# Optimization experiments

Measured on AMD Instinct MI355X. Metric: run time of the kernel, lower is better.

Reference implementation:

```python
import jax, jax.numpy as jnp
from jax import lax
import numpy as np

B, T, F = 32, 512, 512
NUM_OUTPUTS = 23   # joints
DEV_CLASSES = 8
# layer specs: (input_dim, units)
LAYERS = [(F, 1024), (1024, 128), (128, NUM_OUTPUTS),
          (128 + NUM_OUTPUTS, 256), (256, 128), (128, DEV_CLASSES)]


def _gru_params(key, fan_in, units):
    k1, k2, k3 = jax.random.split(key, 3)
    kernel = jax.random.normal(k1, (fan_in, 3 * units), jnp.float32) / jnp.sqrt(jnp.float32(fan_in))
    rkernel = jax.random.normal(k2, (units, 3 * units), jnp.float32) * jnp.float32(0.02)
    bias = jnp.zeros((2, 3 * units), jnp.float32)  # [input_bias, recurrent_bias] (reset_after=True)
    return kernel, rkernel, bias


def setup_inputs() -> dict:
    key = jax.random.key(0)
    keys = jax.random.split(key, 7)
    inp = {"x": jax.random.normal(keys[0], (B, T, F), jnp.float32)}
    for i, (fi, u) in enumerate(LAYERS):
        k, r, b = _gru_params(keys[i + 1], fi, u)
        inp[f"k{i+1}"] = k
        inp[f"r{i+1}"] = r
        inp[f"b{i+1}"] = b
    return inp


def gru(x, kernel, rkernel, bias, act):
    """Keras GRU, reset_after=True, recurrent_activation=sigmoid, gate order z|r|h.
    x: [B,T,F]; kernel: [F,3U]; rkernel: [U,3U]; bias: [2,3U]. Returns [B,T,U]."""
    units = rkernel.shape[0]
    b_i, b_r = bias[0], bias[1]
    # precompute input projections for all timesteps (one big GEMM)
    xp = jnp.einsum('btf,fg->btg', x, kernel) + b_i  # [B,T,3U]

    def step(h, xt):
        rp = h @ rkernel + b_r                       # [B,3U]
        xz, xr, xh = jnp.split(xt, 3, axis=-1)
        rz, rr, rh = jnp.split(rp, 3, axis=-1)
        z = jax.nn.sigmoid(xz + rz)
        r = jax.nn.sigmoid(xr + rr)
        hh = act(xh + r * rh)                        # reset applied AFTER recurrent matmul
        h_new = z * h + (1.0 - z) * hh
        return h_new, h_new

    h0 = jnp.zeros((x.shape[0], units), x.dtype)
    _, ys = lax.scan(step, h0, jnp.swapaxes(xp, 0, 1))  # scan over time
    return jnp.swapaxes(ys, 0, 1)                        # [B,T,U]


relu = jax.nn.relu
linear = lambda v: v


def reference(x, k1, r1, b1, k2, r2, b2, k3, r3, b3,
              k4, r4, b4, k5, r5, b5, k6, r6, b6):
    z = gru(x, k1, r1, b1, relu)          # tcn_gru1: 1024
    z1 = gru(z, k2, r2, b2, relu)         # tcn_gru2: 128
    ye = gru(z1, k3, r3, b3, linear)      # tcn_dgru: num_outputs
    yc = jnp.concatenate([z1, ye], axis=-1)
    y = gru(yc, k4, r4, b4, relu)         # dev_gru1: 256
    y = gru(y, k5, r5, b5, relu)          # dev_gru2: 128
    yd = gru(y, k6, r6, b6, linear)       # dev_dgru: dev_classes
    return ye, yd
```

## Files before the change

kernel.cpp:

```cpp
#include <hip/hip_runtime.h>
#include <hip/hip_bf16.h>
#include <cstdint>
#include <cstddef>

#define BB 32
#define TT 512

typedef short s8v __attribute__((ext_vector_type(8)));
typedef float f4v __attribute__((ext_vector_type(4)));
typedef unsigned long long u64;
typedef unsigned short u16;
typedef unsigned int u32;

__device__ __forceinline__ short f2b(float x) {
  __hip_bfloat16 h = __float2bfloat16(x);
  return *reinterpret_cast<short*>(&h);
}
__device__ __forceinline__ float b2f(u16 x) {
  __hip_bfloat16 h = *reinterpret_cast<__hip_bfloat16*>(&x);
  return __bfloat162float(h);
}
__device__ __forceinline__ float sigm(float x) { return 1.f / (1.f + __expf(-x)); }

__device__ __forceinline__ f4v load16_sc(const void* p) {
  f4v v;
  asm volatile("global_load_dwordx4 %0, %1, off sc0 sc1" : "=v"(v) : "v"(p));
  return v;
}
__device__ __forceinline__ void vm_wait0() {
  asm volatile("s_waitcnt vmcnt(0)" ::: "memory");
}
__device__ __forceinline__ u32 ldP(const u32* p) {
  return __hip_atomic_load(p, __ATOMIC_RELAXED, __HIP_MEMORY_SCOPE_AGENT);
}
__device__ __forceinline__ void stP(u32* p, u32 v) {
  __hip_atomic_store(p, v, __ATOMIC_RELEASE, __HIP_MEMORY_SCOPE_AGENT);
}
__device__ __forceinline__ void stW(u32* p, u32 v) {
  __hip_atomic_store(p, v, __ATOMIC_RELAXED, __HIP_MEMORY_SCOPE_AGENT);
}
__device__ __forceinline__ u32 ldW(const u32* p) {
  return __hip_atomic_load(p, __ATOMIC_RELAXED, __HIP_MEMORY_SCOPE_AGENT);
}

__device__ __forceinline__ void waitP(u32* flags, int baseA, int na, u32 thA,
                                      int baseB, int nbb, u32 thB,
                                      int baseS, int ns, u32 thS) {
  const int tid = threadIdx.x;
  for (;;) {
    int ok = 1;
    if (tid < na) ok = (ldP(&flags[(baseA + tid) * 32]) >= thA) ? 1 : 0;
    else if (tid < na + nbb) ok = (ldP(&flags[(baseB + tid - na) * 32]) >= thB) ? 1 : 0;
    else if (tid < na + nbb + ns) ok = (ldP(&flags[(baseS + tid - na - nbb) * 32]) >= thS) ? 1 : 0;
    if (__syncthreads_count(ok) == (int)blockDim.x) break;
    __builtin_amdgcn_s_sleep(1);
  }
}

__global__ __launch_bounds__(256) void cast_bf16(const float* __restrict__ in,
                                                 u16* __restrict__ outp, int n4) {
  int i = blockIdx.x * 256 + threadIdx.x;
  if (i < n4) {
    float4 v = *(const float4*)(in + (size_t)i * 4);
    u16 o[4] = {(u16)f2b(v.x), (u16)f2b(v.y), (u16)f2b(v.z), (u16)f2b(v.w)};
    *(u64*)(outp + (size_t)i * 4) = *(const u64*)o;
  }
}

__global__ __launch_bounds__(256) void prep_frags(const float* __restrict__ src,
                                                  u16* __restrict__ dst,
                                                  int N, int Ksrc, int Ks,
                                                  int JT, int U, int recmode, int total_fid) {
  int t = blockIdx.x * 256 + threadIdx.x;
  int lane = t & 63, fid = t >> 6;
  if (fid >= total_fid) return;
  int l15 = lane & 15, quad = lane >> 4;
  int ks = fid % Ks;
  int n, valid_n;
  if (recmode) {
    int rest = fid / Ks;
    int jt = rest % JT;
    int g = rest / JT;
    int jj = jt * 16 + l15;
    n = g * U + jj;
    valid_n = (jj < U) ? 1 : 0;
  } else {
    int nt = fid / Ks;
    n = nt * 16 + l15;
    valid_n = (n < N) ? 1 : 0;
  }
  u16* o = dst + ((size_t)fid * 64 + lane) * 8;
#pragma unroll
  for (int j = 0; j < 8; ++j) {
    int k = ks * 32 + quad * 8 + j;
    float v = (valid_n && k < Ksrc) ? src[(size_t)k * N + n] : 0.f;
    o[j] = (u16)f2b(v);
  }
}

__global__ __launch_bounds__(256) void prep_comb(const float* __restrict__ Kmat,
                                                 const float* __restrict__ Rmat,
                                                 u16* __restrict__ dst,
                                                 int N, int U, int w1v, int w1p,
                                                 int w2v, int w2p, int Ks, int JT,
                                                 int total_fid) {
  int t = blockIdx.x * 256 + threadIdx.x;
  int lane = t & 63, fid = t >> 6;
  if (fid >= total_fid) return;
  int l15 = lane & 15, quad = lane >> 4;
  int ks = fid % Ks;
  int rest = fid / Ks;
  int jt = rest % JT;
  int g = rest / JT;
  int j = jt * 16 + l15;
  bool jv = (j < U);
  int n = g * U + (jv ? j : 0);
  u16* o = dst + ((size_t)fid * 64 + lane) * 8;
#pragma unroll
  for (int jj = 0; jj < 8; ++jj) {
    int k = ks * 32 + quad * 8 + jj;
    float v = 0.f;
    if (jv) {
      if (k < w1p) {
        if (k < w1v) v = Kmat[(size_t)k * N + n];
      } else if (k < w1p + w2p) {
        int kr = k - w1p;
        if (kr < w2v) v = Kmat[(size_t)(w1v + kr) * N + n];
      } else {
        int rr = k - w1p - w2p;
        if (rr < U) v = Rmat[(size_t)rr * N + n];
      }
    }
    o[jj] = (u16)f2b(v);
  }
}

__global__ __launch_bounds__(256) void gemm_mfma(const u16* __restrict__ A, int strideA, int Kact,
                                                 const u16* __restrict__ Bf,
                                                 const float* __restrict__ bias,
                                                 float* __restrict__ C,
                                                 int N, int Ntiles, int Ks,
                                                 int t0, int tcLog2) {
  __shared__ char sha[16 * 2056];
  const int tid = threadIdx.x;
  const int lane = tid & 63, l15 = lane & 15, quad = lane >> 4, w = tid >> 6;
  const int KS4 = Ks * 8;
  const int rowB = Ks * 64 + 8;
  const int bm = blockIdx.y * 16;

  for (int i = tid; i < 16 * KS4; i += 256) {
    int r = i / KS4, u = i - r * KS4;
    u64 v = 0;
    if (u * 4 < Kact) {
      int rl = bm + r;
      size_t grow;
      if (t0 >= 0) {
        int tcm = (1 << tcLog2) - 1;
        grow = (((size_t)(rl >> tcLog2)) << 9) + t0 + (rl & tcm);
      } else {
        grow = (size_t)rl;
      }
      v = *((const u64*)(A + grow * (size_t)strideA) + u);
    }
    *(u64*)(sha + r * rowB + u * 8) = v;
  }
  __syncthreads();

  f4v acc[4];
  f4v z4 = {0.f, 0.f, 0.f, 0.f};
#pragma unroll
  for (int q = 0; q < 4; ++q) acc[q] = z4;

  const int ntb = blockIdx.x * 16 + w * 4;
  for (int ks = 0; ks < Ks; ++ks) {
    int off = l15 * rowB + ks * 64 + quad * 16;
    s8v a = *(const s8v*)(sha + off);
#pragma unroll
    for (int q = 0; q < 4; ++q) {
      int nt = ntb + q;
      if (nt < Ntiles) {
        s8v b = *(const s8v*)(Bf + (((size_t)nt * Ks + ks) * 64 + lane) * 8);
        acc[q] = __builtin_amdgcn_mfma_f32_16x16x32_bf16(a, b, acc[q], 0, 0, 0);
      }
    }
  }
#pragma unroll
  for (int q = 0; q < 4; ++q) {
    int nt = ntb + q;
    if (nt >= Ntiles) continue;
    int col = nt * 16 + l15;
    if (col < N) {
      float bv = bias[col];
#pragma unroll
      for (int r = 0; r < 4; ++r) {
        int rowl = bm + quad * 4 + r;
        C[(size_t)rowl * N + col] = acc[q][r] + bv;
      }
    }
  }
}

struct GCfg {
  const u16 *s1, *s2;
  const u16* Bf;
  const float* bias;
  u16* ydst;
  float* fdst;
  u16* hglob;
  int w1p, w2p, Upad, U, Ks, ksIn, JT, nb, base, act, wfd;
  int baseA, na, baseB, nbb;
};

#define SMEM_BYTES 91648
#define HPOFF 74240

__device__ __attribute__((noinline)) void stage_l1(
    const float* xp, const u16* Bf, const float* brec, u16* hbuf, u16* yout,
    u32* flags, int t0, int tc, char* smem) {
  const int tid = threadIdx.x;
  const int lane = tid & 63, l15 = lane & 15, quad = (lane >> 4) & 3;
  const int w = tid >> 6;
  const int blk = blockIdx.x;
  const int jt = blk * 8 + (w & 7);
  const int Mt = w >> 3;
  const int j = jt * 16 + l15;
  const int HP = 32 * 1024;

  const float bz = brec[j], brr = brec[1024 + j], bh = brec[2048 + j];
  float hprev[4];
  {
    const u32* hp = (const u32*)(hbuf + (size_t)(t0 & 1) * HP);
#pragma unroll
    for (int r = 0; r < 4; ++r) {
      int b = Mt * 16 + quad * 4 + r;
      u32 wd = ldW(hp + ((b * 1024 + (j & ~1)) >> 1));
      hprev[r] = b2f((j & 1) ? (u16)(wd >> 16) : (u16)(wd & 0xffff));
    }
  }

  for (int tt = 0; tt < tc; ++tt) {
    const int t = t0 + tt;
    waitP(flags, 0, 8, (u32)t, 0, 0, 0, 0, 0, 0);
    float xv[3][4];
#pragma unroll
    for (int r = 0; r < 4; ++r) {
      int b = Mt * 16 + quad * 4 + r;
      const float* xr_ = xp + ((size_t)b * tc + tt) * 3072;
      xv[0][r] = __builtin_nontemporal_load(xr_ + j);
      xv[1][r] = __builtin_nontemporal_load(xr_ + 1024 + j);
      xv[2][r] = __builtin_nontemporal_load(xr_ + 2048 + j);
    }
    {
      const char* hsrc = (const char*)(hbuf + (size_t)(t & 1) * HP);
      f4v vals[4];
#pragma unroll
      for (int i = 0; i < 4; ++i)
        vals[i] = load16_sc(hsrc + (size_t)(tid + i * 1024) * 16);
      vm_wait0();
#pragma unroll
      for (int i = 0; i < 4; ++i) {
        int g16 = tid + i * 1024;
        *(f4v*)(smem + (g16 >> 7) * 2064 + (g16 & 127) * 16) = vals[i];
      }
    }
    __syncthreads();
    f4v acc[3];
    f4v z4 = {0.f, 0.f, 0.f, 0.f};
#pragma unroll
    for (int g = 0; g < 3; ++g) acc[g] = z4;
#pragma unroll 4
    for (int ks = 0; ks < 32; ++ks) {
      s8v a = *(const s8v*)(smem + (Mt * 16 + l15) * 2064 + ks * 64 + quad * 16);
#pragma unroll
      for (int g = 0; g < 3; ++g) {
        s8v b = *(const s8v*)(Bf + (((size_t)(g * 64 + jt) * 32 + ks) * 64 + lane) * 8);
        acc[g] = __builtin_amdgcn_mfma_f32_16x16x32_bf16(a, b, acc[g], 0, 0, 0);
      }
    }
    u16* hdst = hbuf + (size_t)((t + 1) & 1) * HP;
#pragma unroll
    for (int r = 0; r < 4; ++r) {
      int b = Mt * 16 + quad * 4 + r;
      size_t row = (size_t)b * tc + tt;
      float z = sigm(xv[0][r] + acc[0][r] + bz);
      float rr = sigm(xv[1][r] + acc[1][r] + brr);
      float hh = fmaxf(xv[2][r] + rr * (acc[2][r] + bh), 0.f);
      float hnew = z * hprev[r] + (1.f - z) * hh;
      hprev[r] = hnew;
      float part = __shfl_xor(hnew, 1, 64);
      if ((l15 & 1) == 0) {
        u32 wd = (u32)(u16)f2b(hnew) | ((u32)(u16)f2b(part) << 16);
        stW((u32*)hdst + ((b * 1024 + j) >> 1), wd);
        stW((u32*)yout + ((row * 1024 + j) >> 1), wd);
      }
    }
    __syncthreads();
    if (tid == 0) stP(&flags[blk * 32], (u32)(t + 1));
  }
}

__device__ __attribute__((noinline)) void stage_gen(
    const GCfg& c, int bs, u32* flags, int t0, int tc, int initH, char* smem) {
  const int tid = threadIdx.x;
  const int lane = tid & 63, l15 = lane & 15, quad = (lane >> 4) & 3;
  const int w = tid >> 6;
  const int Kc = c.w1p + c.w2p + c.Upad;
  const int rowA = Kc * 2 + 16;
  const int rowH = c.Upad * 2 + 16;
  char* Ab = smem;
  char* Hp = smem + HPOFF;
  const int HB = 32 * rowH;
  const int uIn = (c.w1p + c.w2p) >> 3;
  const int uH = c.Upad >> 3;
  const int upr = uIn + ((c.nb > 1) ? uH : 0);
  const int total_units = 32 * upr;
  const int u1 = c.w1p >> 3;
  const int U = c.U;
  const int HPstride = 32 * c.Upad;

  const int ntask = c.JT * 2;
  int tcount = 0;
  int tjt[2], tmt[2];
#pragma unroll
  for (int i = 0; i < 2; ++i) {
    int task = w * c.nb + bs + i * 16 * c.nb;
    if (task < ntask) { tjt[tcount] = task >> 1; tmt[tcount] = task & 1; ++tcount; }
  }

  const float* b0 = c.bias;
  const float* b1 = c.bias + 3 * U;
  float bz[2], br_[2], bih[2], brh[2];
  int jl[2];
  bool jv[2];
#pragma unroll
  for (int i = 0; i < 2; ++i) {
    if (i >= tcount) { jv[i] = false; jl[i] = 0; bz[i] = br_[i] = bih[i] = brh[i] = 0.f; continue; }
    int j = tjt[i] * 16 + l15;
    jv[i] = (j < U);
    int jc = jv[i] ? j : 0;
    jl[i] = j;
    bz[i] = b0[jc] + b1[jc];
    br_[i] = b0[U + jc] + b1[U + jc];
    bih[i] = b0[2 * U + jc];
    brh[i] = b1[2 * U + jc];
  }

  if (c.nb == 1) {
    for (int i = tid; i < (2 * HB) >> 2; i += 1024) ((u32*)Hp)[i] = 0;
    __syncthreads();
    if (!initH) {
      for (int i = tid; i < 32 * uH; i += 1024) {
        int m = i / uH, u = i - m * uH;
        *(f4v*)(Hp + (t0 & 1) * HB + m * rowH + u * 16) = *((const f4v*)c.hglob + i);
      }
    }
    __syncthreads();
  }

  float hprev[2][4];
#pragma unroll
  for (int i = 0; i < 2; ++i) {
    if (i >= tcount) continue;
#pragma unroll
    for (int r = 0; r < 4; ++r) {
      int b = tmt[i] * 16 + quad * 4 + r;
      float hv;
      if (c.nb > 1) {
        u32 wd = ldW((const u32*)c.hglob + (((t0 & 1) * HPstride + b * c.Upad + (jl[i] & ~1)) >> 1));
        hv = b2f((jl[i] & 1) ? (u16)(wd >> 16) : (u16)(wd & 0xffff));
      } else {
        hv = b2f(*(const u16*)(Hp + (t0 & 1) * HB + b * rowH + jl[i] * 2));
      }
      hprev[i][r] = jv[i] ? hv : 0.f;
    }
  }

  for (int tt = 0; tt < tc; ++tt) {
    const int t = t0 + tt;
    waitP(flags, c.baseA, c.na, (u32)(t + 1), c.baseB, c.nbb, (u32)(t + 1),
          c.base, (c.nb > 1) ? c.nb : 0, (u32)t);
    {
      f4v vals[5];
      int offs[5];
#pragma unroll
      for (int i = 0; i < 5; ++i) {
        int idx = tid + i * 1024;
        int pidx = (idx < total_units) ? idx : (total_units - 1);
        int m = pidx / upr, u = pidx - m * upr;
        const char* src;
        if (u < u1)
          src = (const char*)c.s1 + ((size_t)(m * tc + tt) * c.w1p + (u << 3)) * 2;
        else if (u < uIn)
          src = (const char*)c.s2 + ((size_t)(m * tc + tt) * c.w2p + ((u - u1) << 3)) * 2;
        else
          src = (const char*)c.hglob + ((size_t)(t & 1) * HPstride + m * c.Upad + ((u - uIn) << 3)) * 2;
        vals[i] = load16_sc(src);
        offs[i] = m * rowA + u * 16;
      }
      vm_wait0();
#pragma unroll
      for (int i = 0; i < 5; ++i)
        if (tid + i * 1024 < total_units) *(f4v*)(Ab + offs[i]) = vals[i];
    }
    __syncthreads();
    f4v az[2], ar[2], axh[2], arh[2];
    f4v z4 = {0.f, 0.f, 0.f, 0.f};
#pragma unroll
    for (int i = 0; i < 2; ++i) { az[i] = z4; ar[i] = z4; axh[i] = z4; arh[i] = z4; }
    for (int ks = 0; ks < c.ksIn; ++ks) {
#pragma unroll
      for (int i = 0; i < 2; ++i) {
        if (i >= tcount) break;
        s8v a = *(const s8v*)(Ab + (tmt[i] * 16 + l15) * rowA + ks * 64 + quad * 16);
        const u16* bb = c.Bf + ((size_t)tjt[i] * c.Ks + ks) * 512 + lane * 8;
        s8v bz_ = *(const s8v*)(bb);
        s8v br2 = *(const s8v*)(bb + (size_t)c.JT * c.Ks * 512);
        s8v bh2 = *(const s8v*)(bb + (size_t)2 * c.JT * c.Ks * 512);
        az[i] = __builtin_amdgcn_mfma_f32_16x16x32_bf16(a, bz_, az[i], 0, 0, 0);
        ar[i] = __builtin_amdgcn_mfma_f32_16x16x32_bf16(a, br2, ar[i], 0, 0, 0);
        axh[i] = __builtin_amdgcn_mfma_f32_16x16x32_bf16(a, bh2, axh[i], 0, 0, 0);
      }
    }
    for (int ks = c.ksIn; ks < c.Ks; ++ks) {
#pragma unroll
      for (int i = 0; i < 2; ++i) {
        if (i >= tcount) break;
        s8v a;
        if (c.nb > 1)
          a = *(const s8v*)(Ab + (tmt[i] * 16 + l15) * rowA + ks * 64 + quad * 16);
        else
          a = *(const s8v*)(Hp + (t & 1) * HB + (tmt[i] * 16 + l15) * rowH + (ks - c.ksIn) * 64 + quad * 16);
        const u16* bb = c.Bf + ((size_t)tjt[i] * c.Ks + ks) * 512 + lane * 8;
        s8v bz_ = *(const s8v*)(bb);
        s8v br2 = *(const s8v*)(bb + (size_t)c.JT * c.Ks * 512);
        s8v bh2 = *(const s8v*)(bb + (size_t)2 * c.JT * c.Ks * 512);
        az[i] = __builtin_amdgcn_mfma_f32_16x16x32_bf16(a, bz_, az[i], 0, 0, 0);
        ar[i] = __builtin_amdgcn_mfma_f32_16x16x32_bf16(a, br2, ar[i], 0, 0, 0);
        arh[i] = __builtin_amdgcn_mfma_f32_16x16x32_bf16(a, bh2, arh[i], 0, 0, 0);
      }
    }
#pragma unroll
    for (int i = 0; i < 2; ++i) {
      if (i >= tcount) break;
#pragma unroll
      for (int r = 0; r < 4; ++r) {
        int b = tmt[i] * 16 + quad * 4 + r;
        size_t row = (size_t)b * tc + tt;
        float z = sigm(az[i][r] + bz[i]);
        float rg = sigm(ar[i][r] + br_[i]);
        float hh = axh[i][r] + bih[i] + rg * (arh[i][r] + brh[i]);
        if (c.act) hh = fmaxf(hh, 0.f);
        float hnew = z * hprev[i][r] + (1.f - z) * hh;
        if (!jv[i]) hnew = 0.f;
        hprev[i][r] = hnew;
        int j = jl[i];
        float part = __shfl_xor(hnew, 1, 64);
        u32 wd = (u32)(u16)f2b(hnew) | ((u32)(u16)f2b(part) << 16);
        if ((l15 & 1) == 0) {
          if (c.ydst) stW((u32*)c.ydst + ((row * c.Upad + j) >> 1), wd);
          if (c.nb > 1)
            stW((u32*)c.hglob + ((((t + 1) & 1) * HPstride + b * c.Upad + j) >> 1), wd);
        }
        if (c.nb == 1) *(u16*)(Hp + ((t + 1) & 1) * HB + b * rowH + j * 2) = (u16)f2b(hnew);
        if (c.fdst && jv[i] && j < c.wfd)
          c.fdst[((size_t)b * TT + t) * c.wfd + j] = hnew;
      }
    }
    __syncthreads();
    if (tid == 0) stP(&flags[(c.base + bs) * 32], (u32)(t + 1));
  }
  if (c.nb == 1) {
    int pf = (t0 + tc) & 1;
    for (int i = tid; i < 32 * uH; i += 1024) {
      int m = i / uH, u = i - m * uH;
      *((f4v*)c.hglob + i) = *(const f4v*)(Hp + pf * HB + m * rowH + u * 16);
    }
  }
}

__global__ __launch_bounds__(1024, 1) void pipeline(
    const float* xp, const u16* BfL1, const float* brecL1, u16* hbufL1, u16* y1c,
    GCfg c1, GCfg c2, GCfg c3, GCfg c4, GCfg c5,
    u32* flags, int t0, int tc, int initH) {
  __shared__ char smem[SMEM_BYTES];
  int blk = blockIdx.x;
  if (blk < 8) stage_l1(xp, BfL1, brecL1, hbufL1, y1c, flags, t0, tc, smem);
  else if (blk < 10) stage_gen(c1, blk - 8, flags, t0, tc, initH, smem);
  else if (blk < 11) stage_gen(c2, 0, flags, t0, tc, initH, smem);
  else if (blk < 13) stage_gen(c3, blk - 11, flags, t0, tc, initH, smem);
  else if (blk < 14) stage_gen(c4, 0, flags, t0, tc, initH, smem);
  else stage_gen(c5, 0, flags, t0, tc, initH, smem);
}

extern "C" void kernel_launch(void* const* d_in, const int* in_sizes, int n_in,
                              void* d_out, int out_size, void* d_ws, size_t ws_size,
                              hipStream_t stream) {
  const float* x = (const float*)d_in[0];

  int tcLog2 = 6;
  {
    size_t fixed = (size_t)16384 * 512 * 2
                   + (3145728ull + 1572864ull + 442368 + 15360 + 319488 + 147456 + 7680) * 2
                   + 300000;
    for (; tcLog2 >= 4; --tcLog2) {
      size_t rc = (size_t)BB << tcLog2;
      size_t per = rc * 3072 * 4 + rc * (1024 + 128 + 32 + 256 + 128) * 2 + 8192;
      if (fixed + per <= ws_size || tcLog2 == 4) break;
    }
  }
  const int Tc = 1 << tcLog2;
  const int NCk = TT / Tc;
  const size_t RC = (size_t)BB * Tc;

  char* ws = (char*)d_ws;
  size_t off = 0;
  auto alloc = [&](size_t bytes) -> char* {
    char* p = ws + off;
    off += (bytes + 255) & ~(size_t)255;
    return p;
  };

  u32* flags = (u32*)alloc(15 * 32 * sizeof(u32));
  u16* hbufL1 = (u16*)alloc((size_t)2 * 32 * 1024 * 2);
  u16* hb2 = (u16*)alloc((size_t)2 * 32 * 128 * 2);
  u16* hb4 = (u16*)alloc((size_t)2 * 32 * 256 * 2);
  u16* hs3 = (u16*)alloc((size_t)32 * 32 * 2);
  u16* hs5 = (u16*)alloc((size_t)32 * 128 * 2);
  u16* hs6 = (u16*)alloc((size_t)32 * 32 * 2);
  u16* recB1 = (u16*)alloc(3145728ull * 2);
  u16* gemB1 = (u16*)alloc(1572864ull * 2);
  u16* cB[5];
  const size_t cBe[5] = {442368, 15360, 319488, 147456, 7680};
  for (int i = 0; i < 5; ++i) cB[i] = (u16*)alloc(cBe[i] * 2);
  u16* x16 = (u16*)alloc((size_t)16384 * 512 * 2);
  float* xp = (float*)alloc(RC * 3072 * sizeof(float));
  u16* y1c = (u16*)alloc(RC * 1024 * 2);
  u16* y2c = (u16*)alloc(RC * 128 * 2);
  u16* yec = (u16*)alloc(RC * 32 * 2);
  u16* y4c = (u16*)alloc(RC * 256 * 2);
  u16* y5c = (u16*)alloc(RC * 128 * 2);

  float* outye = (float*)d_out;
  float* outyd = outye + (size_t)BB * TT * 23;

  hipMemsetAsync(flags, 0, 15 * 32 * sizeof(u32), stream);
  hipMemsetAsync(hbufL1, 0, (size_t)2 * 32 * 1024 * 2, stream);
  hipMemsetAsync(hb2, 0, (size_t)2 * 32 * 128 * 2, stream);
  hipMemsetAsync(hb4, 0, (size_t)2 * 32 * 256 * 2, stream);

  {
    int n4 = (16384 * 512) / 4;
    hipLaunchKernelGGL(cast_bf16, dim3((n4 + 255) / 256), dim3(256), 0, stream, x, x16, n4);
    hipLaunchKernelGGL(prep_frags, dim3((3 * 64 * 32 * 64 + 255) / 256), dim3(256), 0, stream,
                       (const float*)d_in[2], recB1, 3072, 1024, 32, 64, 1024, 1, 3 * 64 * 32);
    hipLaunchKernelGGL(prep_frags, dim3((192 * 16 * 64 + 255) / 256), dim3(256), 0, stream,
                       (const float*)d_in[1], gemB1, 3072, 512, 16, 0, 0, 0, 192 * 16);
    const int pc[5][8] = {
        {384, 128, 1024, 1024, 0, 0, 36, 8},
        {69, 23, 128, 128, 0, 0, 5, 2},
        {768, 256, 128, 128, 23, 32, 13, 16},
        {384, 128, 256, 256, 0, 0, 12, 8},
        {24, 8, 128, 128, 0, 0, 5, 1}};
    for (int i = 0; i < 5; ++i) {
      int l = i + 1;
      int tf = 3 * pc[i][7] * pc[i][6];
      hipLaunchKernelGGL(prep_comb, dim3((tf * 64 + 255) / 256), dim3(256), 0, stream,
                         (const float*)d_in[1 + 3 * l], (const float*)d_in[2 + 3 * l], cB[i],
                         pc[i][0], pc[i][1], pc[i][2], pc[i][3], pc[i][4], pc[i][5],
                         pc[i][6], pc[i][7], tf);
    }
  }

  GCfg c1 = {y1c, nullptr, cB[0], (const float*)d_in[6], y2c, nullptr, hb2,
             1024, 0, 128, 128, 36, 32, 8, 2, 8, 1, 0, 0, 8, 0, 0};
  GCfg c2 = {y2c, nullptr, cB[1], (const float*)d_in[9], yec, outye, hs3,
             128, 0, 32, 23, 5, 4, 2, 1, 10, 0, 23, 8, 2, 0, 0};
  GCfg c3 = {y2c, yec, cB[2], (const float*)d_in[12], y4c, nullptr, hb4,
             128, 32, 256, 256, 13, 5, 16, 2, 11, 1, 0, 8, 2, 10, 1};
  GCfg c4 = {y4c, nullptr, cB[3], (const float*)d_in[15], y5c, nullptr, hs5,
             256, 0, 128, 128, 12, 8, 8, 1, 13, 1, 0, 11, 2, 0, 0};
  GCfg c5 = {y5c, nullptr, cB[4], (const float*)d_in[18], nullptr, outyd, hs6,
             128, 0, 32, 8, 5, 4, 1, 1, 14, 0, 8, 13, 1, 0, 0};

  const float* biasL1 = (const float*)d_in[3];

  for (int c = 0; c < NCk; ++c) {
    const int t0 = c * Tc;
    hipLaunchKernelGGL(gemm_mfma, dim3(12, (unsigned)(RC / 16)), dim3(256), 0, stream,
                       x16, 512, 512, gemB1, biasL1, xp, 3072, 192, 16, t0, tcLog2);
    hipLaunchKernelGGL(pipeline, dim3(15), dim3(1024), 0, stream,
                       xp, recB1, biasL1 + 3072, hbufL1, y1c,
                       c1, c2, c3, c4, c5, flags, t0, Tc, (c == 0) ? 1 : 0);
  }
}
```

Baseline: 15.34 ms.

## Spread GRU pipeline stages over more workgroups with split-K reduction in layer 1

Layer-1 recurrence moves from 8 to 32 workgroups, each owning two 16-column tiles, with the K dimension split across four wave groups and partial sums reduced through shared memory. Downstream stages also get more blocks (c1 8, c3 8, c4 4), and the grid grows to 54 blocks with matching flag/config updates. The flag wait now polls with a single wavefront and then does a block barrier. The aim is to cut per-timestep latency of the serial recurrence by spreading the per-step matmul over more CUs. The cost is more cross-block synchronisation per step, an extra shared-memory reduction, and a larger per-block shared allocation.

```diff
diff --git a/kernel.cpp b/kernel.cpp
--- a/kernel.cpp
+++ b/kernel.cpp
@@ -47,14 +47,17 @@
                                       int baseB, int nbb, u32 thB,
                                       int baseS, int ns, u32 thS) {
   const int tid = threadIdx.x;
-  for (;;) {
-    int ok = 1;
-    if (tid < na) ok = (ldP(&flags[(baseA + tid) * 32]) >= thA) ? 1 : 0;
-    else if (tid < na + nbb) ok = (ldP(&flags[(baseB + tid - na) * 32]) >= thB) ? 1 : 0;
-    else if (tid < na + nbb + ns) ok = (ldP(&flags[(baseS + tid - na - nbb) * 32]) >= thS) ? 1 : 0;
-    if (__syncthreads_count(ok) == (int)blockDim.x) break;
-    __builtin_amdgcn_s_sleep(1);
-  }
+  if (tid < 64) {
+    for (;;) {
+      int ok = 1;
+      if (tid < na) ok = (ldP(&flags[(baseA + tid) * 32]) >= thA) ? 1 : 0;
+      else if (tid < na + nbb) ok = (ldP(&flags[(baseB + tid - na) * 32]) >= thB) ? 1 : 0;
+      else if (tid < na + nbb + ns) ok = (ldP(&flags[(baseS + tid - na - nbb) * 32]) >= thS) ? 1 : 0;
+      if (__all(ok)) break;
+      __builtin_amdgcn_s_sleep(1);
+    }
+  }
+  __syncthreads();
 }
 
 __global__ __launch_bounds__(256) void cast_bf16(const float* __restrict__ in,
@@ -211,7 +214,8 @@
   int baseA, na, baseB, nbb;
 };
 
-#define SMEM_BYTES 91648
+#define REDOFF 66048
+#define SMEM_BYTES 102912
 #define HPOFF 74240
 
 __device__ __attribute__((noinline)) void stage_l1(
@@ -220,15 +224,19 @@
   const int tid = threadIdx.x;
   const int lane = tid & 63, l15 = lane & 15, quad = (lane >> 4) & 3;
   const int w = tid >> 6;
+  const int kq = w >> 2;
+  const int jt_l = (w >> 1) & 1;
+  const int Mt = w & 1;
   const int blk = blockIdx.x;
-  const int jt = blk * 8 + (w & 7);
-  const int Mt = w >> 3;
+  const int jt = blk * 2 + jt_l;
   const int j = jt * 16 + l15;
   const int HP = 32 * 1024;
-
-  const float bz = brec[j], brr = brec[1024 + j], bh = brec[2048 + j];
+  const bool own = (kq == 0);
+
+  float bz = 0.f, brr = 0.f, bh = 0.f;
   float hprev[4];
-  {
+  if (own) {
+    bz = brec[j]; brr = brec[1024 + j]; bh = brec[2048 + j];
     const u32* hp = (const u32*)(hbuf + (size_t)(t0 & 1) * HP);
 #pragma unroll
     for (int r = 0; r < 4; ++r) {
@@ -240,15 +248,17 @@
 
   for (int tt = 0; tt < tc; ++tt) {
     const int t = t0 + tt;
-    waitP(flags, 0, 8, (u32)t, 0, 0, 0, 0, 0, 0);
+    waitP(flags, 0, 32, (u32)t, 0, 0, 0, 0, 0, 0);
     float xv[3][4];
-#pragma unroll
-    for (int r = 0; r < 4; ++r) {
-      int b = Mt * 16 + quad * 4 + r;
-      const float* xr_ = xp + ((size_t)b * tc + tt) * 3072;
-      xv[0][r] = __builtin_nontemporal_load(xr_ + j);
-      xv[1][r] = __builtin_nontemporal_load(xr_ + 1024 + j);
-      xv[2][r] = __builtin_nontemporal_load(xr_ + 2048 + j);
+    if (own) {
+#pragma unroll
+      for (int r = 0; r < 4; ++r) {
+        int b = Mt * 16 + quad * 4 + r;
+        const float* xr_ = xp + ((size_t)b * tc + tt) * 3072;
+        xv[0][r] = __builtin_nontemporal_load(xr_ + j);
+        xv[1][r] = __builtin_nontemporal_load(xr_ + 1024 + j);
+        xv[2][r] = __builtin_nontemporal_load(xr_ + 2048 + j);
+      }
     }
     {
       const char* hsrc = (const char*)(hbuf + (size_t)(t & 1) * HP);
@@ -268,8 +278,9 @@
     f4v z4 = {0.f, 0.f, 0.f, 0.f};
 #pragma unroll
     for (int g = 0; g < 3; ++g) acc[g] = z4;
-#pragma unroll 4
-    for (int ks = 0; ks < 32; ++ks) {
+#pragma unroll
+    for (int i = 0; i < 8; ++i) {
+      int ks = kq * 8 + i;
       s8v a = *(const s8v*)(smem + (Mt * 16 + l15) * 2064 + ks * 64 + quad * 16);
 #pragma unroll
       for (int g = 0; g < 3; ++g) {
@@ -277,21 +288,37 @@
         acc[g] = __builtin_amdgcn_mfma_f32_16x16x32_bf16(a, b, acc[g], 0, 0, 0);
       }
     }
-    u16* hdst = hbuf + (size_t)((t + 1) & 1) * HP;
-#pragma unroll
-    for (int r = 0; r < 4; ++r) {
-      int b = Mt * 16 + quad * 4 + r;
-      size_t row = (size_t)b * tc + tt;
-      float z = sigm(xv[0][r] + acc[0][r] + bz);
-      float rr = sigm(xv[1][r] + acc[1][r] + brr);
-      float hh = fmaxf(xv[2][r] + rr * (acc[2][r] + bh), 0.f);
-      float hnew = z * hprev[r] + (1.f - z) * hh;
-      hprev[r] = hnew;
-      float part = __shfl_xor(hnew, 1, 64);
-      if ((l15 & 1) == 0) {
-        u32 wd = (u32)(u16)f2b(hnew) | ((u32)(u16)f2b(part) << 16);
-        stW((u32*)hdst + ((b * 1024 + j) >> 1), wd);
-        stW((u32*)yout + ((row * 1024 + j) >> 1), wd);
+    if (!own) {
+      int idx = (kq - 1) * 4 + (w & 3);
+#pragma unroll
+      for (int g = 0; g < 3; ++g)
+        *(f4v*)(smem + REDOFF + ((g * 12 + idx) * 64 + lane) * 16) = acc[g];
+    }
+    __syncthreads();
+    if (own) {
+#pragma unroll
+      for (int g = 0; g < 3; ++g)
+#pragma unroll
+        for (int kk = 0; kk < 3; ++kk) {
+          f4v p = *(const f4v*)(smem + REDOFF + ((g * 12 + kk * 4 + w) * 64 + lane) * 16);
+          acc[g] += p;
+        }
+      u16* hdst = hbuf + (size_t)((t + 1) & 1) * HP;
+#pragma unroll
+      for (int r = 0; r < 4; ++r) {
+        int b = Mt * 16 + quad * 4 + r;
+        size_t row = (size_t)b * tc + tt;
+        float z = sigm(xv[0][r] + acc[0][r] + bz);
+        float rr = sigm(xv[1][r] + acc[1][r] + brr);
+        float hh = fmaxf(xv[2][r] + rr * (acc[2][r] + bh), 0.f);
+        float hnew = z * hprev[r] + (1.f - z) * hh;
+        hprev[r] = hnew;
+        float part = __shfl_xor(hnew, 1, 64);
+        if ((l15 & 1) == 0) {
+          u32 wd = (u32)(u16)f2b(hnew) | ((u32)(u16)f2b(part) << 16);
+          stW((u32*)hdst + ((b * 1024 + j) >> 1), wd);
+          stW((u32*)yout + ((row * 1024 + j) >> 1), wd);
+        }
       }
     }
     __syncthreads();
@@ -484,11 +511,11 @@
     u32* flags, int t0, int tc, int initH) {
   __shared__ char smem[SMEM_BYTES];
   int blk = blockIdx.x;
-  if (blk < 8) stage_l1(xp, BfL1, brecL1, hbufL1, y1c, flags, t0, tc, smem);
-  else if (blk < 10) stage_gen(c1, blk - 8, flags, t0, tc, initH, smem);
-  else if (blk < 11) stage_gen(c2, 0, flags, t0, tc, initH, smem);
-  else if (blk < 13) stage_gen(c3, blk - 11, flags, t0, tc, initH, smem);
-  else if (blk < 14) stage_gen(c4, 0, flags, t0, tc, initH, smem);
+  if (blk < 32) stage_l1(xp, BfL1, brecL1, hbufL1, y1c, flags, t0, tc, smem);
+  else if (blk < 40) stage_gen(c1, blk - 32, flags, t0, tc, initH, smem);
+  else if (blk < 41) stage_gen(c2, 0, flags, t0, tc, initH, smem);
+  else if (blk < 49) stage_gen(c3, blk - 41, flags, t0, tc, initH, smem);
+  else if (blk < 53) stage_gen(c4, blk - 49, flags, t0, tc, initH, smem);
   else stage_gen(c5, 0, flags, t0, tc, initH, smem);
 }
 
@@ -520,12 +547,12 @@
     return p;
   };
 
-  u32* flags = (u32*)alloc(15 * 32 * sizeof(u32));
+  u32* flags = (u32*)alloc(54 * 32 * sizeof(u32));
   u16* hbufL1 = (u16*)alloc((size_t)2 * 32 * 1024 * 2);
   u16* hb2 = (u16*)alloc((size_t)2 * 32 * 128 * 2);
   u16* hb4 = (u16*)alloc((size_t)2 * 32 * 256 * 2);
+  u16* hb5 = (u16*)alloc((size_t)2 * 32 * 128 * 2);
   u16* hs3 = (u16*)alloc((size_t)32 * 32 * 2);
-  u16* hs5 = (u16*)alloc((size_t)32 * 128 * 2);
   u16* hs6 = (u16*)alloc((size_t)32 * 32 * 2);
   u16* recB1 = (u16*)alloc(3145728ull * 2);
   u16* gemB1 = (u16*)alloc(1572864ull * 2);
@@ -543,10 +570,11 @@
   float* outye = (float*)d_out;
   float* outyd = outye + (size_t)BB * TT * 23;
 
-  hipMemsetAsync(flags, 0, 15 * 32 * sizeof(u32), stream);
+  hipMemsetAsync(flags, 0, 54 * 32 * sizeof(u32), stream);
   hipMemsetAsync(hbufL1, 0, (size_t)2 * 32 * 1024 * 2, stream);
   hipMemsetAsync(hb2, 0, (size_t)2 * 32 * 128 * 2, stream);
   hipMemsetAsync(hb4, 0, (size_t)2 * 32 * 256 * 2, stream);
+  hipMemsetAsync(hb5, 0, (size_t)2 * 32 * 128 * 2, stream);
 
   {
     int n4 = (16384 * 512) / 4;
@@ -572,15 +600,15 @@
   }
 
   GCfg c1 = {y1c, nullptr, cB[0], (const float*)d_in[6], y2c, nullptr, hb2,
-             1024, 0, 128, 128, 36, 32, 8, 2, 8, 1, 0, 0, 8, 0, 0};
+             1024, 0, 128, 128, 36, 32, 8, 8, 32, 1, 0, 0, 32, 0, 0};
   GCfg c2 = {y2c, nullptr, cB[1], (const float*)d_in[9], yec, outye, hs3,
-             128, 0, 32, 23, 5, 4, 2, 1, 10, 0, 23, 8, 2, 0, 0};
+             128, 0, 32, 23, 5, 4, 2, 1, 40, 0, 23, 32, 8, 0, 0};
   GCfg c3 = {y2c, yec, cB[2], (const float*)d_in[12], y4c, nullptr, hb4,
-             128, 32, 256, 256, 13, 5, 16, 2, 11, 1, 0, 8, 2, 10, 1};
-  GCfg c4 = {y4c, nullptr, cB[3], (const float*)d_in[15], y5c, nullptr, hs5,
-             256, 0, 128, 128, 12, 8, 8, 1, 13, 1, 0, 11, 2, 0, 0};
+             128, 32, 256, 256, 13, 5, 16, 8, 41, 1, 0, 32, 8, 40, 1};
+  GCfg c4 = {y4c, nullptr, cB[3], (const float*)d_in[15], y5c, nullptr, hb5,
+             256, 0, 128, 128, 12, 8, 8, 4, 49, 1, 0, 41, 8, 0, 0};
   GCfg c5 = {y5c, nullptr, cB[4], (const float*)d_in[18], nullptr, outyd, hs6,
-             128, 0, 32, 8, 5, 4, 1, 1, 14, 0, 8, 13, 1, 0, 0};
+             128, 0, 32, 8, 5, 4, 1, 1, 53, 0, 8, 49, 4, 0, 0};
 
   const float* biasL1 = (const float*)d_in[3];
 
@@ -588,7 +616,7 @@
     const int t0 = c * Tc;
     hipLaunchKernelGGL(gemm_mfma, dim3(12, (unsigned)(RC / 16)), dim3(256), 0, stream,
                        x16, 512, 512, gemB1, biasL1, xp, 3072, 192, 16, t0, tcLog2);
-    hipLaunchKernelGGL(pipeline, dim3(15), dim3(1024), 0, stream,
+    hipLaunchKernelGGL(pipeline, dim3(54), dim3(1024), 0, stream,
                        xp, recB1, biasL1 + 3072, hbufL1, y1c,
                        c1, c2, c3, c4, c5, flags, t0, Tc, (c == 0) ? 1 : 0);
   }
```

New measurement: 14.23 ms. 1.08x faster.
